# Optimization experiments

Hardware: AMD Instinct MI355X
Metric: run time of the kernel (lower is better)

Reference implementation:

```python
import jax, jax.numpy as jnp
import numpy as np

GAMMA = 1.0

def _rbf_mean(X, Y, gamma):
    x2 = jnp.sum(X * X, axis=1)  # [n]
    y2 = jnp.sum(Y * Y, axis=1)  # [m]
    d2 = x2[:, None] + y2[None, :] - 2.0 * (X @ Y.T)
    d2 = jnp.maximum(d2, 0.0)
    return jnp.mean(jnp.exp(-gamma * d2))

def setup_inputs() -> dict:
    key = jax.random.key(0)
    k1, k2 = jax.random.split(key)
    N = jax.random.normal(k1, (8192, 256), dtype=jnp.float32)
    R = jax.random.normal(k2, (8192, 256), dtype=jnp.float32)
    return {"N": N, "R": R}

def reference(N, R):
    xx = _rbf_mean(N, N, GAMMA)
    yy = _rbf_mean(R, R, GAMMA)
    xy = _rbf_mean(N, R, GAMMA)
    mmd = xx + yy - 2.0 * xy
    return jnp.sqrt(mmd)
```

## Files before the change

kernel.cpp:

```cpp
#include <hip/hip_runtime.h>
#include <hip/hip_bf16.h>
#include <math.h>

typedef float f32x4 __attribute__((ext_vector_type(4)));
typedef int   i32x4 __attribute__((ext_vector_type(4)));
typedef int   i32x8 __attribute__((ext_vector_type(8)));
typedef float f32x2 __attribute__((ext_vector_type(2)));

#define MTOT 16384
#define HALF 8192
#define KDIM 256
#define BM 128
#define NB (MTOT / BM)
#define NBLK (NB * (NB + 1) / 2)
#define NPART (NBLK * 4)

#define GLDS16(g, l) __builtin_amdgcn_global_load_lds(                      \
    (const __attribute__((address_space(1))) void*)(g),                     \
    (__attribute__((address_space(3))) void*)(l), 16, 0, 0)

__global__ __launch_bounds__(256) void convert_kernel(
    const float* __restrict__ Nmat, const float* __restrict__ Rmat,
    unsigned int* __restrict__ Z, float* __restrict__ x2) {
  const int lane = threadIdx.x & 63;
  const int wv = threadIdx.x >> 6;
  const int row = blockIdx.x * 4 + wv;
  const float* src = (row < HALF) ? (Nmat + (size_t)row * KDIM)
                                  : (Rmat + (size_t)(row - HALF) * KDIM);
  float4 v = *(const float4*)(src + lane * 4);
  int pk = __builtin_amdgcn_cvt_pk_fp8_f32(v.x, v.y, 0, false);
  pk = __builtin_amdgcn_cvt_pk_fp8_f32(v.z, v.w, pk, true);
  Z[(size_t)row * (KDIM / 4) + lane] = (unsigned int)pk;
  f32x2 d01 = __builtin_amdgcn_cvt_pk_f32_fp8(pk, false);
  f32x2 d23 = __builtin_amdgcn_cvt_pk_f32_fp8(pk, true);
  float sq = d01[0] * d01[0] + d01[1] * d01[1] + d23[0] * d23[0] + d23[1] * d23[1];
  #pragma unroll
  for (int off = 32; off; off >>= 1) sq += __shfl_down(sq, off);
  if (lane == 0) x2[row] = sq;
}

__global__ __launch_bounds__(256, 2) void mmd_gemm(
    const unsigned char* __restrict__ Z, const float* __restrict__ x2,
    float* __restrict__ partials) {
  const int t = blockIdx.x;
  const int u = NBLK - 1 - t;
  int rr = (int)((sqrtf(8.0f * (float)u + 1.0f) - 1.0f) * 0.5f);
  while (rr * (rr + 1) / 2 > u) --rr;
  while ((rr + 1) * (rr + 2) / 2 <= u) ++rr;
  const int bm = NB - 1 - rr;
  const int bn = bm + (t - (bm * NB - bm * (bm - 1) / 2));

  __shared__ unsigned char As[BM * KDIM];
  __shared__ unsigned char Bs[BM * KDIM];

  const int tid  = threadIdx.x;
  const int lane = tid & 63;
  const int wid  = tid >> 6;
  const int wm   = wid >> 1;
  const int wn   = wid & 1;

  const unsigned char* Abase = Z + (size_t)bm * BM * KDIM;
  const unsigned char* Bbase = Z + (size_t)bn * BM * KDIM;

  {
    const int lr = lane >> 4;
    const int ls = lane & 15;
    #pragma unroll
    for (int tt = 0; tt < 8; ++tt) {
      int i = wid * 8 + tt;
      int gr = i * 4 + lr;
      int c = ls ^ (gr & 7);
      GLDS16(Abase + (size_t)gr * KDIM + c * 16, As + i * 1024);
      GLDS16(Bbase + (size_t)gr * KDIM + c * 16, Bs + i * 1024);
    }
  }

  const int fr = lane & 15;
  const int fq = lane >> 4;

  float xrh[4][4], xch[4];
  #pragma unroll
  for (int tm = 0; tm < 4; ++tm)
    #pragma unroll
    for (int v = 0; v < 4; ++v)
      xrh[tm][v] = -0.5f * x2[bm * BM + wm * 64 + tm * 16 + fq * 4 + v];
  #pragma unroll
  for (int tn = 0; tn < 4; ++tn)
    xch[tn] = -0.5f * x2[bn * BM + wn * 64 + tn * 16 + fr];

  f32x4 acc[4][4];
  #pragma unroll
  for (int tm = 0; tm < 4; ++tm)
    #pragma unroll
    for (int tn = 0; tn < 4; ++tn)
      #pragma unroll
      for (int v = 0; v < 4; ++v)
        acc[tm][tn][v] = xrh[tm][v] + xch[tn];

  __syncthreads();

  const int key = fr & 7;
  #pragma unroll
  for (int ks = 0; ks < 2; ++ks) {
    const int c0 = ks * 8 + fq * 2;
    i32x8 af[4], bf[4];
    #pragma unroll
    for (int tm = 0; tm < 4; ++tm) {
      int row = wm * 64 + tm * 16 + fr;
      i32x4 lo = *(const i32x4*)(As + row * KDIM + ((c0 ^ key) * 16));
      i32x4 hi = *(const i32x4*)(As + row * KDIM + (((c0 + 1) ^ key) * 16));
      af[tm] = __builtin_shufflevector(lo, hi, 0, 1, 2, 3, 4, 5, 6, 7);
    }
    #pragma unroll
    for (int tn = 0; tn < 4; ++tn) {
      int row = wn * 64 + tn * 16 + fr;
      i32x4 lo = *(const i32x4*)(Bs + row * KDIM + ((c0 ^ key) * 16));
      i32x4 hi = *(const i32x4*)(Bs + row * KDIM + (((c0 + 1) ^ key) * 16));
      bf[tn] = __builtin_shufflevector(lo, hi, 0, 1, 2, 3, 4, 5, 6, 7);
    }
    #pragma unroll
    for (int tm = 0; tm < 4; ++tm)
      #pragma unroll
      for (int tn = 0; tn < 4; ++tn)
        acc[tm][tn] = __builtin_amdgcn_mfma_scale_f32_16x16x128_f8f6f4(
            af[tm], bf[tn], acc[tm][tn], 0, 0,
            0, 0x7F7F7F7F, 0, 0x7F7F7F7F);
  }

  float amax = -1e30f;
  #pragma unroll
  for (int tm = 0; tm < 4; ++tm)
    #pragma unroll
    for (int tn = 0; tn < 4; ++tn)
      #pragma unroll
      for (int v = 0; v < 4; ++v)
        amax = fmaxf(amax, acc[tm][tn][v]);

  float partial = 0.f;
  if (__any(amax > -40.f)) {
    #pragma unroll
    for (int tm = 0; tm < 4; ++tm)
      #pragma unroll
      for (int tn = 0; tn < 4; ++tn)
        #pragma unroll
        for (int v = 0; v < 4; ++v) {
          float a = fminf(acc[tm][tn][v], 0.f);
          partial += exp2f(a * 2.885390082f);
        }
  }

  float wgt = ((bm < NB / 2) == (bn < NB / 2)) ? 1.f : -1.f;
  if (bm != bn) wgt *= 2.f;

  #pragma unroll
  for (int off = 32; off; off >>= 1) partial += __shfl_down(partial, off);
  if (lane == 0) partials[blockIdx.x * 4 + wid] = partial * wgt;
}

__global__ __launch_bounds__(1024) void finalize_kernel(
    const float* __restrict__ partials, float* __restrict__ out) {
  float s = 0.f;
  for (int i = threadIdx.x; i < NPART; i += 1024) s += partials[i];
  #pragma unroll
  for (int off = 32; off; off >>= 1) s += __shfl_down(s, off);
  __shared__ float ws[16];
  if ((threadIdx.x & 63) == 0) ws[threadIdx.x >> 6] = s;
  __syncthreads();
  if (threadIdx.x == 0) {
    float tot = 0.f;
    #pragma unroll
    for (int i = 0; i < 16; ++i) tot += ws[i];
    float mmd = tot / ((float)HALF * (float)HALF);
    out[0] = sqrtf(fmaxf(mmd, 0.f));
  }
}

extern "C" void kernel_launch(void* const* d_in, const int* in_sizes, int n_in,
                              void* d_out, int out_size, void* d_ws, size_t ws_size,
                              hipStream_t stream) {
  const float* Nmat = (const float*)d_in[0];
  const float* Rmat = (const float*)d_in[1];
  float* out = (float*)d_out;

  char* ws = (char*)d_ws;
  unsigned char* Z = (unsigned char*)ws;
  float* x2       = (float*)(ws + (size_t)MTOT * KDIM);
  float* partials = (float*)(ws + (size_t)MTOT * KDIM + MTOT * 4);

  convert_kernel<<<MTOT / 4, 256, 0, stream>>>(Nmat, Rmat, (unsigned int*)Z, x2);
  mmd_gemm<<<NBLK, 256, 0, stream>>>(Z, x2, partials);
  finalize_kernel<<<1, 1024, 0, stream>>>(partials, out);
}
```

Baseline: 122.6 us.

## Use 256x256 tiles with split-K LDS staging and fuse final reduction via atomics

```diff
diff --git a/kernel.cpp b/kernel.cpp
--- a/kernel.cpp
+++ b/kernel.cpp
@@ -1,5 +1,4 @@
 #include <hip/hip_runtime.h>
-#include <hip/hip_bf16.h>
 #include <math.h>
 
 typedef float f32x4 __attribute__((ext_vector_type(4)));
@@ -10,10 +9,9 @@
 #define MTOT 16384
 #define HALF 8192
 #define KDIM 256
-#define BM 128
+#define BM 256
 #define NB (MTOT / BM)
 #define NBLK (NB * (NB + 1) / 2)
-#define NPART (NBLK * 4)
 
 #define GLDS16(g, l) __builtin_amdgcn_global_load_lds(                      \
     (const __attribute__((address_space(1))) void*)(g),                     \
@@ -21,7 +19,9 @@
 
 __global__ __launch_bounds__(256) void convert_kernel(
     const float* __restrict__ Nmat, const float* __restrict__ Rmat,
-    unsigned int* __restrict__ Z, float* __restrict__ x2) {
+    unsigned int* __restrict__ Z, float* __restrict__ x2,
+    float* __restrict__ accum, unsigned int* __restrict__ counter) {
+  if (blockIdx.x == 0 && threadIdx.x == 0) { *accum = 0.f; *counter = 0u; }
   const int lane = threadIdx.x & 63;
   const int wv = threadIdx.x >> 6;
   const int row = blockIdx.x * 4 + wv;
@@ -39,10 +39,11 @@
   if (lane == 0) x2[row] = sq;
 }
 
-__global__ __launch_bounds__(256, 2) void mmd_gemm(
+__global__ __launch_bounds__(512, 2) void mmd_gemm(
     const unsigned char* __restrict__ Z, const float* __restrict__ x2,
-    float* __restrict__ partials) {
-  const int t = blockIdx.x;
+    float* __restrict__ accum, unsigned int* __restrict__ counter,
+    float* __restrict__ out) {
+  const int t = (blockIdx.x & 7) * (NBLK / 8) + (blockIdx.x >> 3);
   const int u = NBLK - 1 - t;
   int rr = (int)((sqrtf(8.0f * (float)u + 1.0f) - 1.0f) * 0.5f);
   while (rr * (rr + 1) / 2 > u) --rr;
@@ -50,86 +51,95 @@
   const int bm = NB - 1 - rr;
   const int bn = bm + (t - (bm * NB - bm * (bm - 1) / 2));
 
-  __shared__ unsigned char As[BM * KDIM];
-  __shared__ unsigned char Bs[BM * KDIM];
+  __shared__ unsigned char As[2 * BM * 128];
+  __shared__ unsigned char Bs[2 * BM * 128];
+  __shared__ float wsred[8];
 
   const int tid  = threadIdx.x;
   const int lane = tid & 63;
   const int wid  = tid >> 6;
-  const int wm   = wid >> 1;
-  const int wn   = wid & 1;
+  const int wm   = wid >> 2;
+  const int wn   = wid & 3;
 
   const unsigned char* Abase = Z + (size_t)bm * BM * KDIM;
   const unsigned char* Bbase = Z + (size_t)bn * BM * KDIM;
 
-  {
-    const int lr = lane >> 4;
-    const int ls = lane & 15;
-    #pragma unroll
-    for (int tt = 0; tt < 8; ++tt) {
-      int i = wid * 8 + tt;
-      int gr = i * 4 + lr;
-      int c = ls ^ (gr & 7);
-      GLDS16(Abase + (size_t)gr * KDIM + c * 16, As + i * 1024);
-      GLDS16(Bbase + (size_t)gr * KDIM + c * 16, Bs + i * 1024);
-    }
+  const int lr = lane >> 3;
+  const int ls = lane & 7;
+  const int cofs = lr * 256 + ((ls ^ lr) << 4);
+
+  #pragma unroll
+  for (int tt = 0; tt < 4; ++tt) {
+    int i = wid * 4 + tt;
+    GLDS16(Abase + i * 2048 + cofs, As + i * 1024);
+    GLDS16(Bbase + i * 2048 + cofs, Bs + i * 1024);
   }
 
   const int fr = lane & 15;
   const int fq = lane >> 4;
 
-  float xrh[4][4], xch[4];
-  #pragma unroll
-  for (int tm = 0; tm < 4; ++tm)
-    #pragma unroll
-    for (int v = 0; v < 4; ++v)
-      xrh[tm][v] = -0.5f * x2[bm * BM + wm * 64 + tm * 16 + fq * 4 + v];
+  float xch[4];
   #pragma unroll
   for (int tn = 0; tn < 4; ++tn)
     xch[tn] = -0.5f * x2[bn * BM + wn * 64 + tn * 16 + fr];
 
-  f32x4 acc[4][4];
-  #pragma unroll
-  for (int tm = 0; tm < 4; ++tm)
+  f32x4 acc[8][4];
+  #pragma unroll
+  for (int tm = 0; tm < 8; ++tm) {
+    float xr[4];
+    #pragma unroll
+    for (int v = 0; v < 4; ++v)
+      xr[v] = -0.5f * x2[bm * BM + wm * 128 + tm * 16 + fq * 4 + v];
     #pragma unroll
     for (int tn = 0; tn < 4; ++tn)
       #pragma unroll
       for (int v = 0; v < 4; ++v)
-        acc[tm][tn][v] = xrh[tm][v] + xch[tn];
+        acc[tm][tn][v] = xr[v] + xch[tn];
+  }
 
   __syncthreads();
 
+  #pragma unroll
+  for (int tt = 0; tt < 4; ++tt) {
+    int i = wid * 4 + tt;
+    GLDS16(Abase + i * 2048 + 128 + cofs, As + 32768 + i * 1024);
+    GLDS16(Bbase + i * 2048 + 128 + cofs, Bs + 32768 + i * 1024);
+  }
+
   const int key = fr & 7;
+  const int slotL = ((2 * fq) ^ key) * 16;
+  const int slotH = ((2 * fq + 1) ^ key) * 16;
+
   #pragma unroll
   for (int ks = 0; ks < 2; ++ks) {
-    const int c0 = ks * 8 + fq * 2;
-    i32x8 af[4], bf[4];
-    #pragma unroll
-    for (int tm = 0; tm < 4; ++tm) {
-      int row = wm * 64 + tm * 16 + fr;
-      i32x4 lo = *(const i32x4*)(As + row * KDIM + ((c0 ^ key) * 16));
-      i32x4 hi = *(const i32x4*)(As + row * KDIM + (((c0 + 1) ^ key) * 16));
-      af[tm] = __builtin_shufflevector(lo, hi, 0, 1, 2, 3, 4, 5, 6, 7);
-    }
+    const unsigned char* A_s = As + ks * 32768;
+    const unsigned char* B_s = Bs + ks * 32768;
+    i32x8 bf[4];
     #pragma unroll
     for (int tn = 0; tn < 4; ++tn) {
       int row = wn * 64 + tn * 16 + fr;
-      i32x4 lo = *(const i32x4*)(Bs + row * KDIM + ((c0 ^ key) * 16));
-      i32x4 hi = *(const i32x4*)(Bs + row * KDIM + (((c0 + 1) ^ key) * 16));
+      i32x4 lo = *(const i32x4*)(B_s + row * 128 + slotL);
+      i32x4 hi = *(const i32x4*)(B_s + row * 128 + slotH);
       bf[tn] = __builtin_shufflevector(lo, hi, 0, 1, 2, 3, 4, 5, 6, 7);
     }
     #pragma unroll
-    for (int tm = 0; tm < 4; ++tm)
+    for (int tm = 0; tm < 8; ++tm) {
+      int row = wm * 128 + tm * 16 + fr;
+      i32x4 lo = *(const i32x4*)(A_s + row * 128 + slotL);
+      i32x4 hi = *(const i32x4*)(A_s + row * 128 + slotH);
+      i32x8 af = __builtin_shufflevector(lo, hi, 0, 1, 2, 3, 4, 5, 6, 7);
       #pragma unroll
       for (int tn = 0; tn < 4; ++tn)
         acc[tm][tn] = __builtin_amdgcn_mfma_scale_f32_16x16x128_f8f6f4(
-            af[tm], bf[tn], acc[tm][tn], 0, 0,
+            af, bf[tn], acc[tm][tn], 0, 0,
             0, 0x7F7F7F7F, 0, 0x7F7F7F7F);
+    }
+    if (ks == 0) __syncthreads();
   }
 
   float amax = -1e30f;
   #pragma unroll
-  for (int tm = 0; tm < 4; ++tm)
+  for (int tm = 0; tm < 8; ++tm)
     #pragma unroll
     for (int tn = 0; tn < 4; ++tn)
       #pragma unroll
@@ -139,7 +149,7 @@
   float partial = 0.f;
   if (__any(amax > -40.f)) {
     #pragma unroll
-    for (int tm = 0; tm < 4; ++tm)
+    for (int tm = 0; tm < 8; ++tm)
       #pragma unroll
       for (int tn = 0; tn < 4; ++tn)
         #pragma unroll
@@ -149,29 +159,25 @@
         }
   }
 
-  float wgt = ((bm < NB / 2) == (bn < NB / 2)) ? 1.f : -1.f;
-  if (bm != bn) wgt *= 2.f;
-
   #pragma unroll
   for (int off = 32; off; off >>= 1) partial += __shfl_down(partial, off);
-  if (lane == 0) partials[blockIdx.x * 4 + wid] = partial * wgt;
-}
-
-__global__ __launch_bounds__(1024) void finalize_kernel(
-    const float* __restrict__ partials, float* __restrict__ out) {
-  float s = 0.f;
-  for (int i = threadIdx.x; i < NPART; i += 1024) s += partials[i];
-  #pragma unroll
-  for (int off = 32; off; off >>= 1) s += __shfl_down(s, off);
-  __shared__ float ws[16];
-  if ((threadIdx.x & 63) == 0) ws[threadIdx.x >> 6] = s;
+  if (lane == 0) wsred[wid] = partial;
   __syncthreads();
-  if (threadIdx.x == 0) {
-    float tot = 0.f;
-    #pragma unroll
-    for (int i = 0; i < 16; ++i) tot += ws[i];
-    float mmd = tot / ((float)HALF * (float)HALF);
-    out[0] = sqrtf(fmaxf(mmd, 0.f));
+
+  if (tid == 0) {
+    float bsum = 0.f;
+    #pragma unroll
+    for (int i = 0; i < 8; ++i) bsum += wsred[i];
+    float wgt = ((bm < NB / 2) == (bn < NB / 2)) ? 1.f : -1.f;
+    if (bm != bn) wgt *= 2.f;
+    atomicAdd(accum, bsum * wgt);
+    __threadfence();
+    unsigned int old = atomicAdd(counter, 1u);
+    if (old == NBLK - 1) {
+      float tot = atomicAdd(accum, 0.f);
+      float mmd = tot / ((float)HALF * (float)HALF);
+      out[0] = sqrtf(fmaxf(mmd, 0.f));
+    }
   }
 }
 
@@ -184,10 +190,11 @@
 
   char* ws = (char*)d_ws;
   unsigned char* Z = (unsigned char*)ws;
-  float* x2       = (float*)(ws + (size_t)MTOT * KDIM);
-  float* partials = (float*)(ws + (size_t)MTOT * KDIM + MTOT * 4);
-
-  convert_kernel<<<MTOT / 4, 256, 0, stream>>>(Nmat, Rmat, (unsigned int*)Z, x2);
-  mmd_gemm<<<NBLK, 256, 0, stream>>>(Z, x2, partials);
-  finalize_kernel<<<1, 1024, 0, stream>>>(partials, out);
+  float* x2        = (float*)(ws + (size_t)MTOT * KDIM);
+  float* accum     = (float*)(ws + (size_t)MTOT * KDIM + (size_t)MTOT * 4);
+  unsigned int* counter = (unsigned int*)(ws + (size_t)MTOT * KDIM + (size_t)MTOT * 4 + 4);
+
+  convert_kernel<<<MTOT / 4, 256, 0, stream>>>(Nmat, Rmat, (unsigned int*)Z, x2,
+                                               accum, counter);
+  mmd_gemm<<<NBLK, 512, 0, stream>>>(Z, x2, accum, counter, out);
 }
```

Result: slower. 139.8 us (+14.0%).
